# Optimization experiments

Hardware: AMD Instinct MI355X
Metric: run time of the kernel (lower is better)

Reference implementation:

```python
import jax, jax.numpy as jnp
import numpy as np

B, C_IN, N = 8, 3, 4096
H = [64, 128, 256]      # local conv widths
G = [128, 64]           # global MLP widths
K = 16                  # kNN neighbors for edge_conv
EPS = 1e-5


def _ln(x, g, b):
    # LayerNorm(num_point): normalize over the last (point) axis per channel
    mu = jnp.mean(x, axis=-1, keepdims=True)
    var = jnp.mean((x - mu) ** 2, axis=-1, keepdims=True)
    return (x - mu) / jnp.sqrt(var + EPS) * g + b


def _conv_ln_relu(x, w, b, g, be):
    # 1x1 Conv1d == per-point matmul: [B,Cin,N] -> [B,Cout,N]
    x = jnp.einsum('oi,bin->bon', w, x) + b[None, :, None]
    return jax.nn.relu(_ln(x, g, be))


def _edge_conv(x):
    # DGCNN-style edge conv: kNN in feature space, max-aggregate neighbor feats
    f = jnp.swapaxes(x, 1, 2)                                  # [B,N,C]
    sq = jnp.sum(f * f, axis=-1)                               # [B,N]
    d = sq[:, :, None] + sq[:, None, :] - 2.0 * jnp.einsum('bnc,bmc->bnm', f, f)
    _, idx = jax.lax.top_k(-jax.lax.stop_gradient(d), K)       # [B,N,K]
    nbr = jax.vmap(lambda fb, ib: fb[ib])(f, idx)              # [B,N,K,C] gather
    return jnp.swapaxes(jnp.max(nbr, axis=2), 1, 2)            # [B,C,N]


def setup_inputs() -> dict:
    key = jax.random.key(0)
    ks = jax.random.split(key, 20)
    inp = {"point_cloud": jax.random.normal(ks[0], (B, C_IN, N), jnp.float32)}
    prev = C_IN
    for i, h in enumerate(H):
        inp[f"w{i}"] = jax.random.normal(ks[1 + 3 * i], (h, prev), jnp.float32) * (1.0 / np.sqrt(prev))
        inp[f"b{i}"] = jnp.zeros((h,), jnp.float32)
        inp[f"g{i}"] = jnp.ones((N,), jnp.float32)
        inp[f"be{i}"] = jnp.zeros((N,), jnp.float32)
        prev = h
    for i, h in enumerate(G + [1]):
        inp[f"gw{i}"] = jax.random.normal(ks[10 + i], (h, prev), jnp.float32) * (1.0 / np.sqrt(prev))
        inp[f"gb{i}"] = jnp.zeros((h,), jnp.float32)
        prev = h
    return inp


def reference(point_cloud, w0, b0, g0, be0, w1, b1, g1, be1, w2, b2, g2, be2,
              gw0, gb0, gw1, gb1, gw2, gb2):
    x = _conv_ln_relu(point_cloud, w0, b0, g0, be0)
    x = _conv_ln_relu(x, w1, b1, g1, be1)
    x = _conv_ln_relu(x, w2, b2, g2, be2)
    x = _edge_conv(x)                      # [B,256,N]
    pooled = jnp.mean(x, axis=2)           # mean over points (pnt_axis=2)
    h = jax.nn.relu(pooled @ gw0.T + gb0)
    h = jax.nn.relu(h @ gw1.T + gb1)
    return h @ gw2.T + gb2                 # [B,1] energy
```

## Files before the change

### kernel.cpp

```cpp
#include <hip/hip_runtime.h>
#include <stdint.h>

#define NPTS 4096
#define BATCH 8
#define KNN 16

typedef __attribute__((ext_vector_type(8))) short short8;
typedef __attribute__((ext_vector_type(4))) float f32x4;
typedef unsigned long long u64;

template<int CIN, int G>
__global__ __launch_bounds__(256) void conv_ln_kernel(
    const float* __restrict__ X, const float* __restrict__ W,
    const float* __restrict__ bias, const float* __restrict__ g,
    const float* __restrict__ be, float* __restrict__ Y, int cout) {
    __shared__ float rows[G * NPTS];
    __shared__ double sh[256], sh2[256];
    int b = blockIdx.x;
    int co0 = blockIdx.y * G;
    int t = threadIdx.x;
    const float* xb = X + (size_t)b * CIN * NPTS;

#pragma unroll 1
    for (int chunk = 0; chunk < 4; ++chunk) {
        int n = chunk * 1024 + t * 4;
        f32x4 acc[G];
#pragma unroll
        for (int j = 0; j < G; ++j) {
            float bj = bias[co0 + j];
            acc[j] = (f32x4){bj, bj, bj, bj};
        }
        for (int ci = 0; ci < CIN; ++ci) {
            f32x4 xv = *(const f32x4*)(xb + (size_t)ci * NPTS + n);
#pragma unroll
            for (int j = 0; j < G; ++j) {
                float w = W[(co0 + j) * CIN + ci];
                acc[j].x = fmaf(w, xv.x, acc[j].x);
                acc[j].y = fmaf(w, xv.y, acc[j].y);
                acc[j].z = fmaf(w, xv.z, acc[j].z);
                acc[j].w = fmaf(w, xv.w, acc[j].w);
            }
        }
#pragma unroll
        for (int j = 0; j < G; ++j)
            *(f32x4*)(rows + j * NPTS + n) = acc[j];
    }
    __syncthreads();

#pragma unroll 1
    for (int j = 0; j < G; ++j) {
        float* row = rows + j * NPTS;
        double s = 0.0, s2 = 0.0;
        for (int i = t * 4; i < NPTS; i += 1024) {
            f32x4 v = *(const f32x4*)(row + i);
            s += (double)v.x + (double)v.y + (double)v.z + (double)v.w;
            s2 += (double)v.x * v.x + (double)v.y * v.y
                + (double)v.z * v.z + (double)v.w * v.w;
        }
        sh[t] = s; sh2[t] = s2;
        __syncthreads();
        for (int off = 128; off > 0; off >>= 1) {
            if (t < off) { sh[t] += sh[t + off]; sh2[t] += sh2[t + off]; }
            __syncthreads();
        }
        double mu = sh[0] / (double)NPTS;
        double var = sh2[0] / (double)NPTS - mu * mu;
        float rstd = (float)(1.0 / sqrt(var + 1e-5));
        float muf = (float)mu;
        float* yrow = Y + ((size_t)b * cout + co0 + j) * NPTS;
        for (int i = t * 4; i < NPTS; i += 1024) {
            f32x4 v = *(const f32x4*)(row + i);
            f32x4 gg = *(const f32x4*)(g + i);
            f32x4 bb = *(const f32x4*)(be + i);
            f32x4 o;
            o.x = fmaxf((v.x - muf) * rstd * gg.x + bb.x, 0.f);
            o.y = fmaxf((v.y - muf) * rstd * gg.y + bb.y, 0.f);
            o.z = fmaxf((v.z - muf) * rstd * gg.z + bb.z, 0.f);
            o.w = fmaxf((v.w - muf) * rstd * gg.w + bb.w, 0.f);
            *(f32x4*)(yrow + i) = o;
        }
        __syncthreads();
    }
}

#define ROW_E 72
#define ROW_B 144

__device__ inline unsigned short f2bf_rne(float x) {
    union { float f; unsigned u; } v; v.f = x;
    unsigned u = v.u;
    return (unsigned short)((u + 0x7FFFu + ((u >> 16) & 1u)) >> 16);
}

__global__ __launch_bounds__(256) void convert_kernel(
    const float* __restrict__ X2, unsigned short* __restrict__ Fc,
    float* __restrict__ SQ, float* __restrict__ Xt) {
    __shared__ float T[64][65];
    __shared__ float Q[64][4];
    int b = blockIdx.y;
    int n0 = blockIdx.x * 64;
    int t = threadIdx.x;
    int n_loc = t >> 2, cq = t & 3;
    int wave = t >> 6, lane = t & 63;
    float sacc = 0.f;
    for (int cc = 0; cc < 4; ++cc) {
        for (int r = 0; r < 16; ++r) {
            int cl = r * 4 + (t >> 6);
            T[cl][t & 63] = X2[((size_t)b * 256 + cc * 64 + cl) * NPTS + n0 + (t & 63)];
        }
        __syncthreads();
        if (Xt) {
#pragma unroll
            for (int r = 0; r < 16; ++r) {
                int n_l = wave * 16 + r;
                Xt[((size_t)b * NPTS + n0 + n_l) * 256 + cc * 64 + lane] = T[lane][n_l];
            }
        }
        size_t base = (((size_t)(b * 4 + cc) * NPTS) + n0 + n_loc) * ROW_E;
#pragma unroll
        for (int j = 0; j < 16; ++j) {
            int c = cq * 16 + j;
            float x = T[c][n_loc];
            sacc = fmaf(x, x, sacc);
            Fc[base + c] = f2bf_rne(x);
        }
        __syncthreads();
    }
    Q[n_loc][cq] = sacc;
    __syncthreads();
    if (t < 64)
        SQ[(size_t)b * NPTS + n0 + t] = Q[t][0] + Q[t][1] + Q[t][2] + Q[t][3];
}

#define A_BYTES (128 * ROW_B)
#define STAGE_BYTES (2 * A_BYTES)
#define SENT32 0xFFFFFFFFu

__device__ inline void async_cp16(const void* g, void* l) {
    __builtin_amdgcn_global_load_lds((const __attribute__((address_space(1))) void*)g,
                                     (__attribute__((address_space(3))) void*)l, 16, 0, 0);
}

__device__ inline unsigned flip_f(float d) {
    union { float f; unsigned u; } v; v.f = d;
    return v.u ^ (((unsigned)((int)v.u >> 31)) | 0x80000000u);
}
__device__ inline float unflip_f(unsigned y) {
    unsigned m = (~((unsigned)((int)y >> 31))) | 0x80000000u;
    union { unsigned u; float f; } v; v.u = y ^ m;
    return v.f;
}
__device__ inline float thr_of(unsigned p) {
    unsigned tb = p | 0xFFFu;
    if (tb >= 0xFF800000u) tb = 0xFF800000u;
    return unflip_f(tb);
}

__global__ __launch_bounds__(256) void knn_mfma_kernel(
    const unsigned short* __restrict__ Fc, const float* __restrict__ SQ,
    unsigned* __restrict__ DpA, unsigned* __restrict__ DpB) {
    __shared__ __align__(16) char smem[STAGE_BYTES];
    __shared__ float sq_ks[128];
    __shared__ float thrx[256];
    int b = blockIdx.x;
    int q0 = blockIdx.y * 128;
    int ks = blockIdx.z;
    int t = threadIdx.x;
    int lane = t & 63;
    int wv = t >> 6;
    int wq = wv & 1, wk = wv >> 1;
    int quad = lane >> 4;
    int l15 = lane & 15;
    const float* sqb = SQ + (size_t)b * NPTS;
    const char* FcB = (const char*)Fc + (size_t)b * 4 * NPTS * ROW_B;

    thrx[t] = __int_as_float(0x7F800000);

    unsigned lst[KNN];
#pragma unroll
    for (int j = 0; j < KNN; ++j) lst[j] = SENT32;
    float thr_part = __int_as_float(0x7F800000);

    int q = t & 127, sub = t >> 7;

    for (int kt = 0; kt < 8; ++kt) {
        int kbase = ks * 1024 + kt * 128;
        if (t < 128) sq_ks[t] = sqb[kbase + t];
        f32x4 acc[4][4];
#pragma unroll
        for (int i = 0; i < 4; ++i)
#pragma unroll
            for (int j = 0; j < 4; ++j) acc[i][j] = (f32x4){0.f, 0.f, 0.f, 0.f};

        for (int kc = 0; kc < 4; ++kc) {
            __syncthreads();
            const char* gA = FcB + ((size_t)kc * NPTS + q0) * ROW_B;
            const char* gB = FcB + ((size_t)kc * NPTS + kbase) * ROW_B;
#pragma unroll
            for (int i = 0; i < 9; ++i) {
                int chunk = (i * 4 + wv) * 1024;
                const char* g = (chunk < A_BYTES) ? (gA + chunk) : (gB + (chunk - A_BYTES));
                async_cp16(g + lane * 16, smem + chunk);
            }
            __syncthreads();
#pragma unroll
            for (int kss = 0; kss < 2; ++kss) {
                int coff = kss * 64 + quad * 16;
                short8 a[4], bf[4];
#pragma unroll
                for (int tq = 0; tq < 4; ++tq)
                    a[tq] = *(const short8*)(smem + (wq * 64 + tq * 16 + l15) * ROW_B + coff);
#pragma unroll
                for (int tk = 0; tk < 4; ++tk)
                    bf[tk] = *(const short8*)(smem + A_BYTES + (wk * 64 + tk * 16 + l15) * ROW_B + coff);
#pragma unroll
                for (int tq = 0; tq < 4; ++tq)
#pragma unroll
                    for (int tk = 0; tk < 4; ++tk)
                        acc[tq][tk] = __builtin_amdgcn_mfma_f32_16x16x32_bf16(
                            a[tq], bf[tk], acc[tq][tk], 0, 0, 0);
            }
        }

        float* Gd = (float*)smem;
        const float* gq = Gd + (size_t)q * 68 + sub * 32;
#pragma unroll 1
        for (int h = 0; h < 2; ++h) {
            __syncthreads();
            if (wk == h) {
#pragma unroll
                for (int tk = 0; tk < 4; ++tk) {
                    float sqk = sq_ks[h * 64 + tk * 16 + l15];
#pragma unroll
                    for (int tq = 0; tq < 4; ++tq) {
                        float* gp = Gd + (size_t)(wq * 64 + tq * 16 + quad * 4) * 68
                                  + tk * 16 + l15;
                        f32x4 g = acc[tq][tk];
                        gp[0]   = fmaf(-2.f, g.x, sqk);
                        gp[68]  = fmaf(-2.f, g.y, sqk);
                        gp[136] = fmaf(-2.f, g.z, sqk);
                        gp[204] = fmaf(-2.f, g.w, sqk);
                    }
                }
            }
            __syncthreads();
            if (h == 0) thr_part = thrx[t ^ 128];
            float thrf = fminf(thr_of(lst[KNN - 1]), thr_part);
            unsigned mask = 0;
#pragma unroll
            for (int i = 7; i >= 0; --i) {
                f32x4 v = *(const f32x4*)(gq + i * 4);
                mask = mask + mask + (unsigned)(v.w <= thrf);
                mask = mask + mask + (unsigned)(v.z <= thrf);
                mask = mask + mask + (unsigned)(v.y <= thrf);
                mask = mask + mask + (unsigned)(v.x <= thrf);
            }
            while (__any((int)(mask != 0u))) {
                if (mask) {
                    int j = __ffs(mask) - 1;
                    mask &= mask - 1u;
                    float d = gq[j];
                    unsigned pk = (flip_f(d) & 0xFFFFF000u)
                                | (unsigned)(kbase + h * 64 + sub * 32 + j);
                    if (pk < lst[KNN - 1]) {
                        lst[KNN - 1] = pk;
#pragma unroll
                        for (int s = KNN - 1; s > 0; --s) {
                            if (lst[s] < lst[s - 1]) {
                                unsigned tmp = lst[s]; lst[s] = lst[s - 1]; lst[s - 1] = tmp;
                            }
                        }
                    }
                }
            }
            if (h == 1) thrx[t] = thr_of(lst[KNN - 1]);
        }
    }

    __syncthreads();
    unsigned* mls = (unsigned*)smem;
#pragma unroll
    for (int j = 0; j < KNN; ++j) mls[t * 17 + j] = lst[j];
    __syncthreads();
    if (t < 128) {
        const unsigned* da = mls + t * 17;
        const unsigned* db = mls + (t + 128) * 17;
        unsigned* outp = ((ks < 2) ? DpA : DpB)
                       + ((size_t)((b * NPTS + q0 + t) * 2 + (ks & 1))) * KNN;
        int ia = 0, ib2 = 0;
        for (int k = 0; k < KNN; ++k) {
            bool ta = (ib2 >= KNN) || (ia < KNN && da[ia] < db[ib2]);
            outp[k] = ta ? da[ia++] : db[ib2++];
        }
    }
}

__global__ __launch_bounds__(256) void transpose_kernel(
    const float* __restrict__ X2, float* __restrict__ Xt) {
    __shared__ float T[64][65];
    int b = blockIdx.x;
    int n0 = blockIdx.y * 64;
    int t = threadIdx.x;
    int wave = t >> 6, lane = t & 63;
    for (int cc = 0; cc < 4; ++cc) {
        for (int r = 0; r < 16; ++r) {
            int cl = r * 4 + (t >> 6);
            T[cl][t & 63] = X2[((size_t)b * 256 + cc * 64 + cl) * NPTS + n0 + (t & 63)];
        }
        __syncthreads();
#pragma unroll
        for (int r = 0; r < 16; ++r) {
            int n_l = wave * 16 + r;
            Xt[((size_t)b * NPTS + n0 + n_l) * 256 + cc * 64 + lane] = T[lane][n_l];
        }
        __syncthreads();
    }
}

__global__ __launch_bounds__(256) void gather_pool_kernel(
    const float* __restrict__ Xt, const unsigned* __restrict__ DpA,
    const unsigned* __restrict__ DpB, float* __restrict__ Pp) {
    __shared__ int idxs[16][KNN];
    int b = blockIdx.x, blk = blockIdx.y;
    int t = threadIdx.x;
    if (t < 16) {
        int qg = b * NPTS + blk * 16 + t;
        const unsigned* L0 = DpA + (size_t)qg * 2 * KNN;
        const unsigned* L1 = L0 + KNN;
        const unsigned* L2 = DpB + (size_t)qg * 2 * KNN;
        const unsigned* L3 = L2 + KNN;
        int p0 = 0, p1 = 0, p2 = 0, p3 = 0;
#pragma unroll 1
        for (int k = 0; k < KNN; ++k) {
            unsigned v0 = (p0 < KNN) ? L0[p0] : SENT32;
            unsigned v1 = (p1 < KNN) ? L1[p1] : SENT32;
            unsigned v2 = (p2 < KNN) ? L2[p2] : SENT32;
            unsigned v3 = (p3 < KNN) ? L3[p3] : SENT32;
            unsigned best = v0; int bl = 0;
            if (v1 < best) { best = v1; bl = 1; }
            if (v2 < best) { best = v2; bl = 2; }
            if (v3 < best) { best = v3; bl = 3; }
            idxs[t][k] = (int)(best & 0xFFFu);
            if (bl == 0) ++p0; else if (bl == 1) ++p1; else if (bl == 2) ++p2; else ++p3;
        }
    }
    __syncthreads();
    int wv = t >> 6, lane = t & 63;
    const float* xb = Xt + (size_t)b * NPTS * 256;
    f32x4 sum = (f32x4){0.f, 0.f, 0.f, 0.f};
#pragma unroll 1
    for (int i = 0; i < 4; ++i) {
        const int* idp = idxs[wv * 4 + i];
        f32x4 m = *(const f32x4*)(xb + (size_t)idp[0] * 256 + lane * 4);
#pragma unroll
        for (int k = 1; k < KNN; ++k) {
            f32x4 v = *(const f32x4*)(xb + (size_t)idp[k] * 256 + lane * 4);
            m.x = fmaxf(m.x, v.x); m.y = fmaxf(m.y, v.y);
            m.z = fmaxf(m.z, v.z); m.w = fmaxf(m.w, v.w);
        }
        sum.x += m.x; sum.y += m.y; sum.z += m.z; sum.w += m.w;
    }
    __shared__ float S[4][256];
    *(f32x4*)&S[wv][lane * 4] = sum;
    __syncthreads();
    Pp[((size_t)b * 256 + blk) * 256 + t] = S[0][t] + S[1][t] + S[2][t] + S[3][t];
}

__global__ __launch_bounds__(256) void pool_mlp_kernel(
    const float* __restrict__ Pp,
    const float* __restrict__ gw0, const float* __restrict__ gb0,
    const float* __restrict__ gw1, const float* __restrict__ gb1,
    const float* __restrict__ gw2, const float* __restrict__ gb2,
    float* __restrict__ out) {
    __shared__ float P[256];
    __shared__ float h1[128];
    __shared__ float h2[64];
    int b = blockIdx.x, t = threadIdx.x;
    double s = 0.0;
#pragma unroll 4
    for (int j = 0; j < 256; ++j) s += (double)Pp[((size_t)b * 256 + j) * 256 + t];
    P[t] = (float)(s / (double)NPTS);
    __syncthreads();
    if (t < 128) {
        const float* w = gw0 + t * 256;
        double acc = 0.0;
        for (int c = 0; c < 256; ++c) acc += (double)P[c] * (double)w[c];
        float v = gb0[t] + (float)acc;
        h1[t] = v > 0.f ? v : 0.f;
    }
    __syncthreads();
    if (t < 64) {
        const float* w = gw1 + t * 128;
        double acc = 0.0;
        for (int c = 0; c < 128; ++c) acc += (double)h1[c] * (double)w[c];
        float v = gb1[t] + (float)acc;
        h2[t] = v > 0.f ? v : 0.f;
    }
    __syncthreads();
    if (t == 0) {
        double acc = 0.0;
        for (int c = 0; c < 64; ++c) acc += (double)h2[c] * (double)gw2[c];
        out[b] = gb2[0] + (float)acc;
    }
}

extern "C" void kernel_launch(void* const* d_in, const int* in_sizes, int n_in,
                              void* d_out, int out_size, void* d_ws, size_t ws_size,
                              hipStream_t stream) {
    const float* pc  = (const float*)d_in[0];
    const float* w0  = (const float*)d_in[1];
    const float* b0  = (const float*)d_in[2];
    const float* g0  = (const float*)d_in[3];
    const float* be0 = (const float*)d_in[4];
    const float* w1  = (const float*)d_in[5];
    const float* b1  = (const float*)d_in[6];
    const float* g1  = (const float*)d_in[7];
    const float* be1 = (const float*)d_in[8];
    const float* w2  = (const float*)d_in[9];
    const float* b2  = (const float*)d_in[10];
    const float* g2  = (const float*)d_in[11];
    const float* be2 = (const float*)d_in[12];
    const float* gw0 = (const float*)d_in[13];
    const float* gb0 = (const float*)d_in[14];
    const float* gw1 = (const float*)d_in[15];
    const float* gb1 = (const float*)d_in[16];
    const float* gw2 = (const float*)d_in[17];
    const float* gb2 = (const float*)d_in[18];
    float* out = (float*)d_out;

    float* ws = (float*)d_ws;
    float* X0 = ws;
    float* X2 = X0 + 2097152;
    float* R  = X2 + 8388608;
    float* X1 = R;
    unsigned short* Fc = (unsigned short*)R;
    unsigned* DpA = (unsigned*)X0;
    unsigned* DpB = (unsigned*)(R + 9437184);
    float* SQ = R + 11534336;
    float* P  = SQ + 32768;
    float* Pp = P + 2048;
    float* Xt2 = Pp + 524288;

    bool roomy = ws_size >= (size_t)(22579200ull + 8388608ull) * 4ull;
    float* Xt = roomy ? Xt2 : R;

    conv_ln_kernel<3, 2><<<dim3(BATCH, 64 / 2), 256, 0, stream>>>(
        pc, w0, b0, g0, be0, X0, 64);
    conv_ln_kernel<64, 4><<<dim3(BATCH, 128 / 4), 256, 0, stream>>>(
        X0, w1, b1, g1, be1, X1, 128);
    conv_ln_kernel<128, 4><<<dim3(BATCH, 256 / 4), 256, 0, stream>>>(
        X1, w2, b2, g2, be2, X2, 256);

    convert_kernel<<<dim3(NPTS / 64, BATCH), 256, 0, stream>>>(
        X2, Fc, SQ, roomy ? Xt2 : nullptr);
    knn_mfma_kernel<<<dim3(BATCH, 32, 4), 256, 0, stream>>>(Fc, SQ, DpA, DpB);
    if (!roomy)
        transpose_kernel<<<dim3(BATCH, NPTS / 64), 256, 0, stream>>>(X2, Xt);
    gather_pool_kernel<<<dim3(BATCH, 256), 256, 0, stream>>>(Xt, DpA, DpB, Pp);
    pool_mlp_kernel<<<dim3(BATCH), 256, 0, stream>>>(Pp, gw0, gb0, gw1, gb1, gw2, gb2, out);
}
```

Before: 482.1 us.

## Double-buffer LDS tile loads in kNN MFMA kernel to overlap copy and compute

Replaces the single-stage LDS staging in the kNN distance kernel with two buffers. The next (kt,kc) tile is prefetched with async global-to-LDS copies while MFMAs run on the current buffer, and a prologue issues the first tile before the loop. This removes one barrier per inner step and reuses the idle buffer for the distance scratch tile. The cost is doubled LDS usage, which may lower blocks per CU, and the async-copy wait before each barrier may limit how much overlap is actually achieved.

New measurement: 475.7 us, median of 2. No clear change (-1.3%).

```diff
diff --git a/kernel.cpp b/kernel.cpp
--- a/kernel.cpp
+++ b/kernel.cpp
@@ -132,8 +132,8 @@
         SQ[(size_t)b * NPTS + n0 + t] = Q[t][0] + Q[t][1] + Q[t][2] + Q[t][3];
 }
 
-#define A_BYTES (128 * ROW_B)
-#define STAGE_BYTES (2 * A_BYTES)
+#define A_BYTES 18432
+#define BUF_B   36864
 #define SENT32 0xFFFFFFFFu
 
 __device__ inline void async_cp16(const void* g, void* l) {
@@ -159,7 +159,7 @@
 __global__ __launch_bounds__(256) void knn_mfma_kernel(
     const unsigned short* __restrict__ Fc, const float* __restrict__ SQ,
     unsigned* __restrict__ DpA, unsigned* __restrict__ DpB) {
-    __shared__ __align__(16) char smem[STAGE_BYTES];
+    __shared__ __align__(16) char smem[2 * BUF_B];
     __shared__ float sq_ks[128];
     __shared__ float thrx[256];
     int b = blockIdx.x;
@@ -183,6 +183,18 @@
 
     int q = t & 127, sub = t >> 7;
 
+    {
+        const char* gA = FcB + (size_t)q0 * ROW_B;
+        const char* gB = FcB + (size_t)(ks * 1024) * ROW_B;
+#pragma unroll
+        for (int i = 0; i < 9; ++i) {
+            int chunk = (i * 4 + wv) * 1024;
+            const char* g = (chunk < A_BYTES) ? (gA + chunk) : (gB + (chunk - A_BYTES));
+            async_cp16(g + lane * 16, smem + chunk);
+        }
+    }
+    __syncthreads();
+
     for (int kt = 0; kt < 8; ++kt) {
         int kbase = ks * 1024 + kt * 128;
         if (t < 128) sq_ks[t] = sqb[kbase + t];
@@ -192,27 +204,33 @@
 #pragma unroll
             for (int j = 0; j < 4; ++j) acc[i][j] = (f32x4){0.f, 0.f, 0.f, 0.f};
 
+#pragma unroll 1
         for (int kc = 0; kc < 4; ++kc) {
-            __syncthreads();
-            const char* gA = FcB + ((size_t)kc * NPTS + q0) * ROW_B;
-            const char* gB = FcB + ((size_t)kc * NPTS + kbase) * ROW_B;
-#pragma unroll
-            for (int i = 0; i < 9; ++i) {
-                int chunk = (i * 4 + wv) * 1024;
-                const char* g = (chunk < A_BYTES) ? (gA + chunk) : (gB + (chunk - A_BYTES));
-                async_cp16(g + lane * 16, smem + chunk);
-            }
-            __syncthreads();
+            int g = kt * 4 + kc;
+            int gn = g + 1;
+            if (gn < 32) {
+                int kcn = gn & 3, ktn = gn >> 2;
+                const char* gA = FcB + ((size_t)kcn * NPTS + q0) * ROW_B;
+                const char* gB = FcB + ((size_t)kcn * NPTS + ks * 1024 + ktn * 128) * ROW_B;
+                char* dst = smem + (gn & 1) * BUF_B;
+#pragma unroll
+                for (int i = 0; i < 9; ++i) {
+                    int chunk = (i * 4 + wv) * 1024;
+                    const char* gp = (chunk < A_BYTES) ? (gA + chunk) : (gB + (chunk - A_BYTES));
+                    async_cp16(gp + lane * 16, dst + chunk);
+                }
+            }
+            const char* base = smem + (g & 1) * BUF_B;
 #pragma unroll
             for (int kss = 0; kss < 2; ++kss) {
                 int coff = kss * 64 + quad * 16;
                 short8 a[4], bf[4];
 #pragma unroll
                 for (int tq = 0; tq < 4; ++tq)
-                    a[tq] = *(const short8*)(smem + (wq * 64 + tq * 16 + l15) * ROW_B + coff);
+                    a[tq] = *(const short8*)(base + (wq * 64 + tq * 16 + l15) * ROW_B + coff);
 #pragma unroll
                 for (int tk = 0; tk < 4; ++tk)
-                    bf[tk] = *(const short8*)(smem + A_BYTES + (wk * 64 + tk * 16 + l15) * ROW_B + coff);
+                    bf[tk] = *(const short8*)(base + A_BYTES + (wk * 64 + tk * 16 + l15) * ROW_B + coff);
 #pragma unroll
                 for (int tq = 0; tq < 4; ++tq)
 #pragma unroll
@@ -220,13 +238,13 @@
                         acc[tq][tk] = __builtin_amdgcn_mfma_f32_16x16x32_bf16(
                             a[tq], bf[tk], acc[tq][tk], 0, 0, 0);
             }
-        }
-
-        float* Gd = (float*)smem;
+            __syncthreads();
+        }
+
+        float* Gd = (float*)(smem + BUF_B);
         const float* gq = Gd + (size_t)q * 68 + sub * 32;
 #pragma unroll 1
         for (int h = 0; h < 2; ++h) {
-            __syncthreads();
             if (wk == h) {
 #pragma unroll
                 for (int tk = 0; tk < 4; ++tk) {
@@ -274,10 +292,10 @@
                 }
             }
             if (h == 1) thrx[t] = thr_of(lst[KNN - 1]);
-        }
-    }
-
-    __syncthreads();
+            __syncthreads();
+        }
+    }
+
     unsigned* mls = (unsigned*)smem;
 #pragma unroll
     for (int j = 0; j < KNN; ++j) mls[t * 17 + j] = lst[j];
```
